# Performance work log

Measured on AMD Instinct MI355X. Metric: run time of the kernel, lower is better.

Reference implementation:

```python
import jax, jax.numpy as jnp
import numpy as np

EPS = 1e-5

def _ln(x, g, b):
    mu = jnp.mean(x, axis=-1, keepdims=True)
    var = jnp.var(x, axis=-1, keepdims=True)
    return (x - mu) * jax.lax.rsqrt(var + EPS) * g + b

def setup_inputs() -> dict:
    key = jax.random.key(0)
    ks = jax.random.split(key, 8)
    B, N, D, H = 1, 512, 128, 128
    s = 1.0 / np.sqrt(D)
    inp = {
        'x': jax.random.normal(ks[0], (B, N, N, D), dtype=jnp.float32),
        'src_mask': jax.random.randint(ks[1], (B, N), 0, 2, dtype=jnp.int32),
        'ln_g': jnp.ones((D,), jnp.float32), 'ln_b': jnp.zeros((D,), jnp.float32),
        'Wl': jax.random.normal(ks[2], (D, H), jnp.float32) * s,
        'bl': jnp.zeros((H,), jnp.float32),
        'Wr': jax.random.normal(ks[3], (D, H), jnp.float32) * s,
        'br': jnp.zeros((H,), jnp.float32),
        # gates: faithful to nn.init.constant_(weight, 0.), constant_(bias, 1.)
        'Wlg': jnp.zeros((D, H), jnp.float32), 'blg': jnp.ones((H,), jnp.float32),
        'Wrg': jnp.zeros((D, H), jnp.float32), 'brg': jnp.ones((H,), jnp.float32),
        'Wog': jnp.zeros((D, H), jnp.float32), 'bog': jnp.ones((H,), jnp.float32),
        'oln_g': jnp.ones((H,), jnp.float32), 'oln_b': jnp.zeros((H,), jnp.float32),
        'Wo': jax.random.normal(ks[4], (H, D), jnp.float32) / np.sqrt(H),
        'bo': jnp.zeros((D,), jnp.float32),
    }
    return inp

def reference(x, src_mask, ln_g, ln_b, Wl, bl, Wr, br, Wlg, blg, Wrg, brg, Wog, bog, oln_g, oln_b, Wo, bo):
    # pairwise mask (B,i,j,1) = outer product of src_mask with itself
    m = src_mask.astype(jnp.float32)
    mask = (m[:, :, None] * m[:, None, :])[..., None]
    xn = _ln(x, ln_g, ln_b)
    # original applies left/right proj to detached xn (no grad to x via these paths)
    xd = jax.lax.stop_gradient(xn)
    left = (xd @ Wl + bl) * mask
    right = (xd @ Wr + br) * mask
    left = left * jax.nn.sigmoid(xn @ Wlg + blg)
    right = right * jax.nn.sigmoid(xn @ Wrg + brg)
    out_gate = jax.nn.sigmoid(xn @ Wog + bog)
    # ingoing mix: '... k j d, ... k i d -> ... i j d'
    out = jnp.einsum('bkjd,bkid->bijd', left, right)
    out = _ln(out, oln_g, oln_b) * out_gate
    return out @ Wo + bo
```

## Files before the change

kernel.cpp:

```cpp
#include <hip/hip_runtime.h>
#include <stdint.h>

#define NN 512
#define PP (NN * NN)

typedef __attribute__((ext_vector_type(8))) short bf16x8;
typedef __attribute__((ext_vector_type(4))) float f32x4;

#define MFMA16 __builtin_amdgcn_mfma_f32_16x16x32_bf16

__device__ __forceinline__ unsigned short f2bf(float f) {
  unsigned u = __float_as_uint(f);
  u += 0x7fffu + ((u >> 16) & 1u);
  return (unsigned short)(u >> 16);
}
__device__ __forceinline__ float bf2f(unsigned short s) {
  return __uint_as_float(((unsigned)s) << 16);
}
__device__ __forceinline__ unsigned pack2(float a, float b) {
  return (unsigned)f2bf(a) | ((unsigned)f2bf(b) << 16);
}
__device__ __forceinline__ float sigm(float t) { return 1.0f / (1.0f + __expf(-t)); }

__device__ __forceinline__ int sidx(int p, int h) {
  return p * 136 + (h ^ (((p >> 3) & 7) << 3));
}

__global__ __launch_bounds__(256) void k_prep(
    const float* __restrict__ w0, const float* __restrict__ w1,
    const float* __restrict__ w2, const float* __restrict__ w3,
    const float* __restrict__ w4, const float* __restrict__ w5,
    unsigned short* __restrict__ outw) {
  const float* src;
  switch (blockIdx.x) {
    case 0: src = w0; break; case 1: src = w1; break; case 2: src = w2; break;
    case 3: src = w3; break; case 4: src = w4; break; default: src = w5; break;
  }
  unsigned short* o = outw + blockIdx.x * 16384;
  for (int idx = threadIdx.x; idx < 16384; idx += 256) {
    int r = idx >> 7, c = idx & 127;
    o[idx] = f2bf(src[c * 128 + r]);
  }
}

__global__ __launch_bounds__(256) void k_ln(
    const float* __restrict__ x, const float* __restrict__ g,
    const float* __restrict__ b, unsigned short* __restrict__ xn) {
  const int lane = threadIdx.x & 63, wid = threadIdx.x >> 6;
  const int row = blockIdx.x * 32 + wid * 8 + (lane >> 3);
  const int ch = lane & 7;
  const float4* xr = (const float4*)(x + (size_t)row * 128 + ch * 16);
  float4 V[4];
  float s = 0.f, ss = 0.f;
#pragma unroll
  for (int q = 0; q < 4; ++q) {
    V[q] = xr[q];
    s  += V[q].x + V[q].y + V[q].z + V[q].w;
    ss += V[q].x * V[q].x + V[q].y * V[q].y + V[q].z * V[q].z + V[q].w * V[q].w;
  }
#pragma unroll
  for (int o = 1; o < 8; o <<= 1) { s += __shfl_xor(s, o); ss += __shfl_xor(ss, o); }
  float mu  = s * 0.0078125f;
  float var = ss * 0.0078125f - mu * mu;
  float rs  = rsqrtf(var + 1e-5f);
  const float4* gp = (const float4*)(g + ch * 16);
  const float4* bp = (const float4*)(b + ch * 16);
  unsigned pk[8];
#pragma unroll
  for (int q = 0; q < 4; ++q) {
    float4 vv = V[q], gg = gp[q], bb = bp[q];
    pk[2 * q]     = pack2((vv.x - mu) * rs * gg.x + bb.x, (vv.y - mu) * rs * gg.y + bb.y);
    pk[2 * q + 1] = pack2((vv.z - mu) * rs * gg.z + bb.z, (vv.w - mu) * rs * gg.w + bb.w);
  }
  unsigned short* dst = xn + (size_t)row * 128 + ch * 16;
  *(uint4*)dst       = make_uint4(pk[0], pk[1], pk[2], pk[3]);
  *(uint4*)(dst + 8) = make_uint4(pk[4], pk[5], pk[6], pk[7]);
}

__global__ __launch_bounds__(256) void k_proj(
    const unsigned short* __restrict__ xn,
    const unsigned short* __restrict__ WpT, const float* __restrict__ bp,
    const unsigned short* __restrict__ WgT, const float* __restrict__ bg,
    const int* __restrict__ mask,
    unsigned short* __restrict__ outb) {
  const int c  = blockIdx.y;
  const int k0 = blockIdx.x * 128;
  const int t = threadIdx.x, lane = t & 63, wid = t >> 6;
  const int wm = (wid >> 1) * 64, wn = (wid & 1) * 64;
  const int lr = lane & 15, lg = lane >> 4;
  __shared__ unsigned short sX[128 * 136];
  __shared__ unsigned short sW[128 * 136];

#pragma unroll
  for (int it = 0; it < 8; ++it) {
    int lin = it * 256 + t;
    int r = lin >> 4, ch = lin & 15;
    *(uint4*)&sX[r * 136 + ch * 8] =
        *(const uint4*)&xn[((size_t)(k0 + r) * NN + c) * 128 + ch * 8];
  }
#pragma unroll
  for (int it = 0; it < 8; ++it) {
    int lin = it * 256 + t;
    *(uint4*)&sW[(lin >> 4) * 136 + (lin & 15) * 8] = *(const uint4*)&WgT[lin * 8];
  }
  __syncthreads();

  f32x4 acc[4][4];
#pragma unroll
  for (int m = 0; m < 4; ++m)
#pragma unroll
    for (int n = 0; n < 4; ++n) { acc[m][n][0] = 0.f; acc[m][n][1] = 0.f; acc[m][n][2] = 0.f; acc[m][n][3] = 0.f; }

#pragma unroll
  for (int kk = 0; kk < 4; ++kk) {
    bf16x8 av[4], bv[4];
#pragma unroll
    for (int m = 0; m < 4; ++m)
      av[m] = *(const bf16x8*)&sW[(wm + m * 16 + lr) * 136 + kk * 32 + lg * 8];
#pragma unroll
    for (int n = 0; n < 4; ++n)
      bv[n] = *(const bf16x8*)&sX[(wn + n * 16 + lr) * 136 + kk * 32 + lg * 8];
#pragma unroll
    for (int m = 0; m < 4; ++m)
#pragma unroll
      for (int n = 0; n < 4; ++n)
        acc[m][n] = MFMA16(av[m], bv[n], acc[m][n], 0, 0, 0);
  }
  float sg[4][4][4];
#pragma unroll
  for (int m = 0; m < 4; ++m)
#pragma unroll
    for (int r = 0; r < 4; ++r) {
      int h = wm + m * 16 + lg * 4 + r;
      float bgv = bg[h];
#pragma unroll
      for (int n = 0; n < 4; ++n) sg[m][n][r] = sigm(acc[m][n][r] + bgv);
    }
  __syncthreads();
#pragma unroll
  for (int it = 0; it < 8; ++it) {
    int lin = it * 256 + t;
    *(uint4*)&sW[(lin >> 4) * 136 + (lin & 15) * 8] = *(const uint4*)&WpT[lin * 8];
  }
  __syncthreads();

#pragma unroll
  for (int m = 0; m < 4; ++m)
#pragma unroll
    for (int n = 0; n < 4; ++n) { acc[m][n][0] = 0.f; acc[m][n][1] = 0.f; acc[m][n][2] = 0.f; acc[m][n][3] = 0.f; }
#pragma unroll
  for (int kk = 0; kk < 4; ++kk) {
    bf16x8 av[4], bv[4];
#pragma unroll
    for (int m = 0; m < 4; ++m)
      av[m] = *(const bf16x8*)&sW[(wm + m * 16 + lr) * 136 + kk * 32 + lg * 8];
#pragma unroll
    for (int n = 0; n < 4; ++n)
      bv[n] = *(const bf16x8*)&sX[(wn + n * 16 + lr) * 136 + kk * 32 + lg * 8];
#pragma unroll
    for (int m = 0; m < 4; ++m)
#pragma unroll
      for (int n = 0; n < 4; ++n)
        acc[m][n] = MFMA16(av[m], bv[n], acc[m][n], 0, 0, 0);
  }

  const int maskc = mask[c];
  float mcol[4];
#pragma unroll
  for (int n = 0; n < 4; ++n)
    mcol[n] = (float)(maskc * mask[k0 + wn + n * 16 + lr]);
#pragma unroll
  for (int m = 0; m < 4; ++m)
#pragma unroll
    for (int r = 0; r < 4; ++r) {
      int h = wm + m * 16 + lg * 4 + r;
      float bpv = bp[h];
#pragma unroll
      for (int n = 0; n < 4; ++n) {
        float v = (acc[m][n][r] + bpv) * mcol[n] * sg[m][n][r];
        outb[(size_t)h * PP + (size_t)c * NN + k0 + wn + n * 16 + lr] = f2bf(v);
      }
    }
}

__global__ __launch_bounds__(256) void k_einsum(
    const unsigned short* __restrict__ rightT,
    const unsigned short* __restrict__ leftT,
    unsigned short* __restrict__ tmp) {
  const int d = blockIdx.z;
  const int i0 = blockIdx.y * 128, j0 = blockIdx.x * 128;
  const unsigned short* A = rightT + (size_t)d * PP;
  const unsigned short* B = leftT + (size_t)d * PP;
  const int t = threadIdx.x, lane = t & 63, wid = t >> 6;
  const int wm = (wid >> 1) * 64, wn = (wid & 1) * 64;
  const int lr = lane & 15, lg = lane >> 4;
  __shared__ unsigned short sA[128 * 72];
  __shared__ unsigned short sB[128 * 72];

  f32x4 acc[4][4];
#pragma unroll
  for (int m = 0; m < 4; ++m)
#pragma unroll
    for (int n = 0; n < 4; ++n) { acc[m][n][0] = 0.f; acc[m][n][1] = 0.f; acc[m][n][2] = 0.f; acc[m][n][3] = 0.f; }

  for (int kb = 0; kb < 8; ++kb) {
#pragma unroll
    for (int it = 0; it < 4; ++it) {
      int lin = it * 256 + t;
      int r = lin >> 3, ch = lin & 7;
      *(uint4*)&sA[r * 72 + ch * 8] =
          *(const uint4*)&A[(size_t)(i0 + r) * NN + kb * 64 + ch * 8];
      *(uint4*)&sB[r * 72 + ch * 8] =
          *(const uint4*)&B[(size_t)(j0 + r) * NN + kb * 64 + ch * 8];
    }
    __syncthreads();
#pragma unroll
    for (int kk = 0; kk < 2; ++kk) {
      bf16x8 av[4], bv[4];
#pragma unroll
      for (int m = 0; m < 4; ++m)
        av[m] = *(const bf16x8*)&sA[(wm + m * 16 + lr) * 72 + kk * 32 + lg * 8];
#pragma unroll
      for (int n = 0; n < 4; ++n)
        bv[n] = *(const bf16x8*)&sB[(wn + n * 16 + lr) * 72 + kk * 32 + lg * 8];
#pragma unroll
      for (int m = 0; m < 4; ++m)
#pragma unroll
        for (int n = 0; n < 4; ++n)
          acc[m][n] = MFMA16(av[m], bv[n], acc[m][n], 0, 0, 0);
    }
    __syncthreads();
  }
#pragma unroll
  for (int m = 0; m < 4; ++m)
#pragma unroll
    for (int r = 0; r < 4; ++r) {
      int row = wm + m * 16 + lg * 4 + r;
#pragma unroll
      for (int n = 0; n < 4; ++n) {
        int col = wn + n * 16 + lr;
        tmp[(size_t)d * PP + (size_t)(i0 + row) * NN + j0 + col] = f2bf(acc[m][n][r]);
      }
    }
}

__global__ __launch_bounds__(256, 2) void k_final(
    const unsigned short* __restrict__ xn,
    const unsigned short* __restrict__ WogT, const float* __restrict__ bog,
    const unsigned short* __restrict__ WoT, const float* __restrict__ bo,
    const unsigned short* __restrict__ tmp,
    const float* __restrict__ og, const float* __restrict__ ob,
    float* __restrict__ out) {
  const int p0 = blockIdx.x * 128;
  const int t = threadIdx.x, lane = t & 63, wid = t >> 6;
  const int wm = (wid >> 1) * 64, wn = (wid & 1) * 64;
  const int lr = lane & 15, lg = lane >> 4;
  __shared__ unsigned short sT[128 * 136];
  __shared__ unsigned short sSig[128 * 136];
  __shared__ float muL[128], rsL[128];

#pragma unroll 8
  for (int it = 0; it < 32; ++it) {
    int lin = it * 256 + t;
    int h = lin >> 6, pc = lin & 63;
    unsigned u = *(const unsigned*)&tmp[(size_t)h * PP + p0 + pc * 2];
    sT[sidx(pc * 2, h)]     = (unsigned short)(u & 0xffffu);
    sT[sidx(pc * 2 + 1, h)] = (unsigned short)(u >> 16);
  }

  f32x4 acc[4][4];
#pragma unroll
  for (int m = 0; m < 4; ++m)
#pragma unroll
    for (int n = 0; n < 4; ++n) { acc[m][n][0] = 0.f; acc[m][n][1] = 0.f; acc[m][n][2] = 0.f; acc[m][n][3] = 0.f; }
#pragma unroll
  for (int kk = 0; kk < 4; ++kk) {
    bf16x8 av[4], bv[4];
#pragma unroll
    for (int m = 0; m < 4; ++m)
      av[m] = *(const bf16x8*)&xn[(size_t)(p0 + wm + m * 16 + lr) * 128 + kk * 32 + lg * 8];
#pragma unroll
    for (int n = 0; n < 4; ++n)
      bv[n] = *(const bf16x8*)&WogT[(wn + n * 16 + lr) * 128 + kk * 32 + lg * 8];
#pragma unroll
    for (int m = 0; m < 4; ++m)
#pragma unroll
      for (int n = 0; n < 4; ++n)
        acc[m][n] = MFMA16(av[m], bv[n], acc[m][n], 0, 0, 0);
  }
  float bogv[4];
#pragma unroll
  for (int n = 0; n < 4; ++n) bogv[n] = bog[wn + n * 16 + lr];
#pragma unroll
  for (int m = 0; m < 4; ++m)
#pragma unroll
    for (int r = 0; r < 4; ++r) {
      int p = wm + m * 16 + lg * 4 + r;
#pragma unroll
      for (int n = 0; n < 4; ++n)
        sSig[sidx(p, wn + n * 16 + lr)] = f2bf(sigm(acc[m][n][r] + bogv[n]));
    }
  __syncthreads();

  {
    int p = t >> 1, half = t & 1;
    float s = 0.f, ss = 0.f;
#pragma unroll
    for (int c = 0; c < 8; ++c) {
      bf16x8 v = *(const bf16x8*)&sT[sidx(p, half * 64 + c * 8)];
#pragma unroll
      for (int e = 0; e < 8; ++e) {
        float f = bf2f((unsigned short)v[e]);
        s += f; ss += f * f;
      }
    }
    s += __shfl_xor(s, 1); ss += __shfl_xor(ss, 1);
    if (half == 0) {
      float mu = s * 0.0078125f;
      float var = ss * 0.0078125f - mu * mu;
      muL[p] = mu;
      rsL[p] = rsqrtf(var + 1e-5f);
    }
  }
  __syncthreads();

#pragma unroll
  for (int m = 0; m < 4; ++m)
#pragma unroll
    for (int n = 0; n < 4; ++n) { acc[m][n][0] = 0.f; acc[m][n][1] = 0.f; acc[m][n][2] = 0.f; acc[m][n][3] = 0.f; }
#pragma unroll
  for (int kk = 0; kk < 4; ++kk) {
    const int h0 = kk * 32 + lg * 8;
    float ogv[8], obv[8];
    *(float4*)&ogv[0] = *(const float4*)&og[h0];
    *(float4*)&ogv[4] = *(const float4*)&og[h0 + 4];
    *(float4*)&obv[0] = *(const float4*)&ob[h0];
    *(float4*)&obv[4] = *(const float4*)&ob[h0 + 4];
    bf16x8 av[4], bv[4];
#pragma unroll
    for (int m = 0; m < 4; ++m) {
      int p = wm + m * 16 + lr;
      float mu = muL[p], rr = rsL[p];
      bf16x8 tv = *(const bf16x8*)&sT[sidx(p, h0)];
      bf16x8 gv = *(const bf16x8*)&sSig[sidx(p, h0)];
      bf16x8 y;
#pragma unroll
      for (int e = 0; e < 8; ++e) {
        float tf = bf2f((unsigned short)tv[e]);
        float yf = ((tf - mu) * rr * ogv[e] + obv[e]) * bf2f((unsigned short)gv[e]);
        y[e] = (short)f2bf(yf);
      }
      av[m] = y;
    }
#pragma unroll
    for (int n = 0; n < 4; ++n)
      bv[n] = *(const bf16x8*)&WoT[(wn + n * 16 + lr) * 128 + h0];
#pragma unroll
    for (int m = 0; m < 4; ++m)
#pragma unroll
      for (int n = 0; n < 4; ++n)
        acc[m][n] = MFMA16(av[m], bv[n], acc[m][n], 0, 0, 0);
  }

  float bov[4];
#pragma unroll
  for (int n = 0; n < 4; ++n) bov[n] = bo[wn + n * 16 + lr];
#pragma unroll
  for (int m = 0; m < 4; ++m)
#pragma unroll
    for (int r = 0; r < 4; ++r) {
      int p = wm + m * 16 + lg * 4 + r;
#pragma unroll
      for (int n = 0; n < 4; ++n)
        out[(size_t)(p0 + p) * 128 + wn + n * 16 + lr] = acc[m][n][r] + bov[n];
    }
}

extern "C" void kernel_launch(void* const* d_in, const int* in_sizes, int n_in,
                              void* d_out, int out_size, void* d_ws, size_t ws_size,
                              hipStream_t stream) {
  (void)in_sizes; (void)n_in; (void)out_size;
  const float* x    = (const float*)d_in[0];
  const int*   msk  = (const int*)d_in[1];
  const float* ln_g = (const float*)d_in[2];
  const float* ln_b = (const float*)d_in[3];
  const float* Wl   = (const float*)d_in[4];
  const float* bl   = (const float*)d_in[5];
  const float* Wr   = (const float*)d_in[6];
  const float* br   = (const float*)d_in[7];
  const float* Wlg  = (const float*)d_in[8];
  const float* blg  = (const float*)d_in[9];
  const float* Wrg  = (const float*)d_in[10];
  const float* brg  = (const float*)d_in[11];
  const float* Wog  = (const float*)d_in[12];
  const float* bog  = (const float*)d_in[13];
  const float* olng = (const float*)d_in[14];
  const float* olnb = (const float*)d_in[15];
  const float* Wo   = (const float*)d_in[16];
  const float* bo   = (const float*)d_in[17];
  float* out = (float*)d_out;

  const size_t need = (1ull << 20) + 4ull * (1ull << 26);
  if (ws_size < need) return;
  char* ws = (char*)d_ws;
  unsigned short* wT    = (unsigned short*)ws;
  unsigned short* xn    = (unsigned short*)(ws + (1ull << 20));
  unsigned short* leftT = (unsigned short*)(ws + (1ull << 20) + (1ull << 26));
  unsigned short* rightT= (unsigned short*)(ws + (1ull << 20) + (2ull << 26));
  unsigned short* tmp   = (unsigned short*)(ws + (1ull << 20) + (3ull << 26));

  hipLaunchKernelGGL(k_prep, dim3(6), dim3(256), 0, stream, Wl, Wr, Wlg, Wrg, Wog, Wo, wT);
  hipLaunchKernelGGL(k_ln, dim3(PP / 32), dim3(256), 0, stream, x, ln_g, ln_b, xn);
  hipLaunchKernelGGL(k_proj, dim3(4, NN), dim3(256), 0, stream,
                     xn, wT + 0 * 16384, bl, wT + 2 * 16384, blg, msk, leftT);
  hipLaunchKernelGGL(k_proj, dim3(4, NN), dim3(256), 0, stream,
                     xn, wT + 1 * 16384, br, wT + 3 * 16384, brg, msk, rightT);
  hipLaunchKernelGGL(k_einsum, dim3(4, 4, 128), dim3(256), 0, stream, rightT, leftT, tmp);
  hipLaunchKernelGGL(k_final, dim3(PP / 128), dim3(256), 0, stream,
                     xn, wT + 4 * 16384, bog, wT + 5 * 16384, bo, tmp, olng, olnb, out);
}
```

Before: 300.2 us.

## Enlarge einsum tiles to 256x256 with 512 threads, vectorize final transpose load

The batched einsum GEMM moves from 128x128 tiles with 256 threads to 256x256 tiles with 512 threads, using a flattened, swizzled block index. Each warp now computes 128x64, which halves global and LDS reloads per output, but 128 accumulator registers per thread may lower occupancy. The k_final transpose load now gathers 8 channels per thread and writes them to LDS as one 16-byte vector instead of scalar shorts. Per-row LayerNorm mean and rstd are also hoisted from LDS into registers before the loop that uses them.

```diff
diff --git a/kernel.cpp b/kernel.cpp
--- a/kernel.cpp
+++ b/kernel.cpp
@@ -183,30 +183,31 @@
     }
 }
 
-__global__ __launch_bounds__(256) void k_einsum(
+__global__ __launch_bounds__(512) void k_einsum(
     const unsigned short* __restrict__ rightT,
     const unsigned short* __restrict__ leftT,
     unsigned short* __restrict__ tmp) {
-  const int d = blockIdx.z;
-  const int i0 = blockIdx.y * 128, j0 = blockIdx.x * 128;
+  const int bid = (blockIdx.x & 7) * 64 + (blockIdx.x >> 3);
+  const int d = bid >> 2;
+  const int i0 = ((bid >> 1) & 1) * 256, j0 = (bid & 1) * 256;
   const unsigned short* A = rightT + (size_t)d * PP;
   const unsigned short* B = leftT + (size_t)d * PP;
   const int t = threadIdx.x, lane = t & 63, wid = t >> 6;
-  const int wm = (wid >> 1) * 64, wn = (wid & 1) * 64;
+  const int wm = (wid >> 2) * 128, wn = (wid & 3) * 64;
   const int lr = lane & 15, lg = lane >> 4;
-  __shared__ unsigned short sA[128 * 72];
-  __shared__ unsigned short sB[128 * 72];
-
-  f32x4 acc[4][4];
-#pragma unroll
-  for (int m = 0; m < 4; ++m)
+  __shared__ unsigned short sA[256 * 72];
+  __shared__ unsigned short sB[256 * 72];
+
+  f32x4 acc[8][4];
+#pragma unroll
+  for (int m = 0; m < 8; ++m)
 #pragma unroll
     for (int n = 0; n < 4; ++n) { acc[m][n][0] = 0.f; acc[m][n][1] = 0.f; acc[m][n][2] = 0.f; acc[m][n][3] = 0.f; }
 
   for (int kb = 0; kb < 8; ++kb) {
 #pragma unroll
     for (int it = 0; it < 4; ++it) {
-      int lin = it * 256 + t;
+      int lin = it * 512 + t;
       int r = lin >> 3, ch = lin & 7;
       *(uint4*)&sA[r * 72 + ch * 8] =
           *(const uint4*)&A[(size_t)(i0 + r) * NN + kb * 64 + ch * 8];
@@ -216,23 +217,22 @@
     __syncthreads();
 #pragma unroll
     for (int kk = 0; kk < 2; ++kk) {
-      bf16x8 av[4], bv[4];
-#pragma unroll
-      for (int m = 0; m < 4; ++m)
-        av[m] = *(const bf16x8*)&sA[(wm + m * 16 + lr) * 72 + kk * 32 + lg * 8];
+      bf16x8 bv[4];
 #pragma unroll
       for (int n = 0; n < 4; ++n)
         bv[n] = *(const bf16x8*)&sB[(wn + n * 16 + lr) * 72 + kk * 32 + lg * 8];
 #pragma unroll
-      for (int m = 0; m < 4; ++m)
+      for (int m = 0; m < 8; ++m) {
+        bf16x8 av = *(const bf16x8*)&sA[(wm + m * 16 + lr) * 72 + kk * 32 + lg * 8];
 #pragma unroll
         for (int n = 0; n < 4; ++n)
-          acc[m][n] = MFMA16(av[m], bv[n], acc[m][n], 0, 0, 0);
+          acc[m][n] = MFMA16(av, bv[n], acc[m][n], 0, 0, 0);
+      }
     }
     __syncthreads();
   }
 #pragma unroll
-  for (int m = 0; m < 4; ++m)
+  for (int m = 0; m < 8; ++m)
 #pragma unroll
     for (int r = 0; r < 4; ++r) {
       int row = wm + m * 16 + lg * 4 + r;
@@ -259,13 +259,24 @@
   __shared__ unsigned short sSig[128 * 136];
   __shared__ float muL[128], rsL[128];
 
-#pragma unroll 8
-  for (int it = 0; it < 32; ++it) {
-    int lin = it * 256 + t;
-    int h = lin >> 6, pc = lin & 63;
-    unsigned u = *(const unsigned*)&tmp[(size_t)h * PP + p0 + pc * 2];
-    sT[sidx(pc * 2, h)]     = (unsigned short)(u & 0xffffu);
-    sT[sidx(pc * 2 + 1, h)] = (unsigned short)(u >> 16);
+  {
+    const int pb = 2 * lane;
+#pragma unroll
+    for (int q = 0; q < 4; ++q) {
+      int h0 = (q * 4 + wid) * 8;
+      unsigned a[8];
+#pragma unroll
+      for (int e = 0; e < 8; ++e)
+        a[e] = *(const unsigned*)&tmp[(size_t)(h0 + e) * PP + p0 + pb];
+      bf16x8 y0, y1;
+#pragma unroll
+      for (int e = 0; e < 8; ++e) {
+        y0[e] = (short)(a[e] & 0xffffu);
+        y1[e] = (short)(a[e] >> 16);
+      }
+      *(bf16x8*)&sT[sidx(pb, h0)]     = y0;
+      *(bf16x8*)&sT[sidx(pb + 1, h0)] = y1;
+    }
   }
 
   f32x4 acc[4][4];
@@ -328,6 +339,12 @@
   for (int m = 0; m < 4; ++m)
 #pragma unroll
     for (int n = 0; n < 4; ++n) { acc[m][n][0] = 0.f; acc[m][n][1] = 0.f; acc[m][n][2] = 0.f; acc[m][n][3] = 0.f; }
+  float muR[4], rsR[4];
+#pragma unroll
+  for (int m = 0; m < 4; ++m) {
+    int p = wm + m * 16 + lr;
+    muR[m] = muL[p]; rsR[m] = rsL[p];
+  }
 #pragma unroll
   for (int kk = 0; kk < 4; ++kk) {
     const int h0 = kk * 32 + lg * 8;
@@ -340,7 +357,7 @@
 #pragma unroll
     for (int m = 0; m < 4; ++m) {
       int p = wm + m * 16 + lr;
-      float mu = muL[p], rr = rsL[p];
+      float mu = muR[m], rr = rsR[m];
       bf16x8 tv = *(const bf16x8*)&sT[sidx(p, h0)];
       bf16x8 gv = *(const bf16x8*)&sSig[sidx(p, h0)];
       bf16x8 y;
@@ -415,7 +432,7 @@
                      xn, wT + 0 * 16384, bl, wT + 2 * 16384, blg, msk, leftT);
   hipLaunchKernelGGL(k_proj, dim3(4, NN), dim3(256), 0, stream,
                      xn, wT + 1 * 16384, br, wT + 3 * 16384, brg, msk, rightT);
-  hipLaunchKernelGGL(k_einsum, dim3(4, 4, 128), dim3(256), 0, stream, rightT, leftT, tmp);
+  hipLaunchKernelGGL(k_einsum, dim3(512), dim3(512), 0, stream, rightT, leftT, tmp);
   hipLaunchKernelGGL(k_final, dim3(PP / 128), dim3(256), 0, stream,
                      xn, wT + 4 * 16384, bog, wT + 5 * 16384, bo, tmp, olng, olnb, out);
 }
```

Result: faster. 274.5 us (-8.6%).
